# Optimization experiments

Measured on AMD Instinct MI355X. Metric: run time of the kernel, lower is better.

The kernel has to match this reference:

```python
import jax, jax.numpy as jnp
import numpy as np

PAD = 1
K = 3  # kernel_size


def conv2d(x, w, b):
    y = jax.lax.conv_general_dilated(
        x, w, window_strides=(1, 1), padding=((PAD, PAD), (PAD, PAD)),
        dimension_numbers=("NCHW", "OIHW", "NCHW"))
    return y + b[None, :, None, None]


def deform_conv2d(x, offset, weight, bias):
    # torchvision.ops.deform_conv2d semantics (stride=1, dilation=1, 1 offset group)
    B, C, H, W = x.shape
    O = weight.shape[0]
    K2 = K * K
    off = offset.reshape(B, K2, 2, H, W)  # [...,0]=dy, [...,1]=dx
    ky, kx = jnp.meshgrid(jnp.arange(K), jnp.arange(K), indexing="ij")
    ky = ky.reshape(K2).astype(x.dtype)
    kx = kx.reshape(K2).astype(x.dtype)
    hh = jnp.arange(H, dtype=x.dtype)
    ww = jnp.arange(W, dtype=x.dtype)
    # sampling coords, shape [B, K2, H, W]
    py = off[:, :, 0] + ky[None, :, None, None] + hh[None, None, :, None] - PAD
    px = off[:, :, 1] + kx[None, :, None, None] + ww[None, None, None, :] - PAD

    y0 = jnp.floor(py)
    x0 = jnp.floor(px)
    wy = (py - y0)[:, None]  # [B,1,K2,H,W]
    wx = (px - x0)[:, None]

    xf = x.reshape(B, C, H * W)

    def gather(iy, ix):
        valid = (iy >= 0) & (iy < H) & (ix >= 0) & (ix < W)
        iyc = jnp.clip(iy, 0, H - 1).astype(jnp.int32)
        ixc = jnp.clip(ix, 0, W - 1).astype(jnp.int32)
        idx = (iyc * W + ixc).reshape(B, 1, K2 * H * W)
        v = jnp.take_along_axis(xf, idx, axis=2).reshape(B, C, K2, H, W)
        return v * valid.reshape(B, 1, K2, H, W).astype(x.dtype)

    v00 = gather(y0, x0)
    v01 = gather(y0, x0 + 1)
    v10 = gather(y0 + 1, x0)
    v11 = gather(y0 + 1, x0 + 1)
    sampled = (v00 * (1 - wy) * (1 - wx) + v01 * (1 - wy) * wx
               + v10 * wy * (1 - wx) + v11 * wy * wx)  # [B,C,K2,H,W]
    out = jnp.einsum("bckhw,ock->bohw", sampled, weight.reshape(O, C, K2))
    return out + bias[None, :, None, None]


def setup_inputs() -> dict:
    key = jax.random.key(0)
    k1, k2, k3, k4, k5 = jax.random.split(key, 5)
    B, C, H, W = 4, 64, 192, 192
    O = 64
    x = jax.random.normal(k1, (B, C, H, W), dtype=jnp.float32)
    w_off = jax.random.normal(k2, (2 * K * K, C, K, K), dtype=jnp.float32) * 0.05
    b_off = jnp.zeros((2 * K * K,), dtype=jnp.float32)
    w_conv = jax.random.normal(k3, (O, C, K, K), dtype=jnp.float32) * (1.0 / np.sqrt(C * K * K))
    b_conv = jax.random.normal(k4, (O,), dtype=jnp.float32) * 0.01
    return {"x": x, "w_off": w_off, "b_off": b_off, "w_conv": w_conv, "b_conv": b_conv}


def reference(x, w_off, b_off, w_conv, b_conv):
    offset = conv2d(x, w_off, b_off)
    y = deform_conv2d(x, offset, w_conv, b_conv)
    return conv2d(y, w_conv, b_conv)  # module reuses self.conv on deform output
```

## Files before the change

### kernel.cpp

```cpp
#include <hip/hip_runtime.h>

constexpr int B = 4;
constexpr int C = 64;
constexpr int O = 64;
constexpr int OOFF = 18;
constexpr int H = 192;
constexpr int W = 192;

typedef __attribute__((ext_vector_type(8))) _Float16 half8;
typedef __attribute__((ext_vector_type(2))) _Float16 h16x2;
typedef __attribute__((ext_vector_type(4))) float float4v;

__device__ inline ushort f2h(float f) {
  return __builtin_bit_cast(ushort, (_Float16)f);
}
__device__ inline uint pk2h(float lo, float hi) {
  h16x2 v;
  v.x = (_Float16)lo;
  v.y = (_Float16)hi;
  return __builtin_bit_cast(uint, v);
}

__global__ __launch_bounds__(256) void k_pre(const float* __restrict__ x,
                                             ushort* __restrict__ xtf,
                                             const float* __restrict__ w_conv,
                                             ushort* __restrict__ wBf,
                                             const float* __restrict__ w_off,
                                             ushort* __restrict__ wOf) {
  __shared__ float tile[64][17];
  const int bid = blockIdx.x;
  const int tid = threadIdx.x;
  if (bid < 9216) {
    const int w0 = (bid % 12) * 16;
    const int h = (bid / 12) % 192;
    const int b = bid / 2304;
    const int wl = tid & 15;
    const int c0 = tid >> 4;
#pragma unroll
    for (int r = 0; r < 4; ++r) {
      const int c = c0 + r * 16;
      tile[c][wl] = x[(((size_t)b * C + c) * H + h) * W + w0 + wl];
    }
    __syncthreads();
    const int c = tid & 63;
    const int qq = tid >> 6;
#pragma unroll
    for (int r = 0; r < 4; ++r) {
      const int wq = qq + r * 4;
      xtf[(((size_t)b * H + h) * W + w0 + wq) * C + c] = f2h(tile[c][wq]);
    }
  } else if (bid < 9360) {
    const int i = (bid - 9216) * 256 + tid;
    const int j = i & 7;
    const int lane = (i >> 3) & 63;
    const int nt = (i >> 9) & 3;
    const int kstep = (i >> 11) & 1;
    const int kk = i >> 12;
    const int n = nt + 4 * (lane & 15);
    const int c = kstep * 32 + ((lane >> 4) & 3) * 8 + j;
    wBf[i] = f2h(w_conv[((size_t)n * C + c) * 9 + kk]);
  } else {
    const int i = (bid - 9360) * 256 + tid;
    const int j = i & 7;
    const int lane = (i >> 3) & 63;
    const int nt = (i >> 9) & 1;
    const int ks = (i >> 10) & 1;
    const int kk = i >> 11;
    const int n = nt * 16 + (lane & 15);
    const int c = ks * 32 + ((lane >> 4) & 3) * 8 + j;
    wOf[i] = (n < OOFF) ? f2h(w_off[((size_t)n * C + c) * 9 + kk]) : (ushort)0;
  }
}

__global__ __launch_bounds__(256) void k_fused(
    const ushort* __restrict__ xtf, const ushort* __restrict__ wOf,
    const float* __restrict__ b_off, const ushort* __restrict__ wBf,
    const float* __restrict__ b_conv, ushort* __restrict__ yt) {
  __shared__ ushort sA[4][2][64][8];
  __shared__ __align__(16) float offBuf[4][16][20];

  const int bid = blockIdx.x;
  const int xcd = bid & 7;
  const int s = bid >> 3;
  const int b = xcd >> 1;
  const int half = xcd & 1;
  const int th = half * 12 + s / 24;
  const int tw = s % 24;
  const int h0 = th * 8, w0 = tw * 8;

  const int tid = threadIdx.x;
  const int wave = tid >> 6, lane = tid & 63;
  const int col = lane & 15, quad = lane >> 4;
  const int p = tid >> 2, qtr = tid & 3;
  const int pl = p & 15;
  const int prow = p >> 3, pcol = p & 7;
  const int h = h0 + prow, w = w0 + pcol;
  const int ks_w = qtr >> 1;
  const int q2 = (qtr & 1) * 2;

  {
    float4v oacc[2];
#pragma unroll
    for (int nt = 0; nt < 2; ++nt) oacc[nt] = (float4v){0.f, 0.f, 0.f, 0.f};

    half8 obfr[2][2][2];
    half8 oafr[2][2];

    auto oload = [&](int kk, int pb) {
      const int ky = kk / 3, kx = kk % 3;
      const int hh = h0 + 2 * wave + (col >> 3) + ky - 1;
      const int ww = w0 + (col & 7) + kx - 1;
      const bool ok = ((unsigned)hh < (unsigned)H) && ((unsigned)ww < (unsigned)W);
      const int hhc = min(max(hh, 0), H - 1);
      const int wwc = min(max(ww, 0), W - 1);
      const ushort* pa = xtf + (((size_t)b * H + hhc) * W + wwc) * C + quad * 8;
#pragma unroll
      for (int ks = 0; ks < 2; ++ks) {
        half8 v = (half8)0;
        if (ok) v = *(const half8*)(pa + ks * 32);
        oafr[pb][ks] = v;
#pragma unroll
        for (int nt = 0; nt < 2; ++nt)
          obfr[pb][ks][nt] = *(const half8*)&wOf[((((size_t)kk * 2 + ks) * 2 + nt) * 64 + lane) * 8];
      }
    };

    oload(0, 0);
#pragma unroll
    for (int kk = 0; kk < 9; ++kk) {
      const int pb = kk & 1;
      if (kk < 8) oload(kk + 1, pb ^ 1);
#pragma unroll
      for (int ks = 0; ks < 2; ++ks)
#pragma unroll
        for (int nt = 0; nt < 2; ++nt)
          oacc[nt] = __builtin_amdgcn_mfma_f32_16x16x32_f16(oafr[pb][ks], obfr[pb][ks][nt],
                                                            oacc[nt], 0, 0, 0);
    }

#pragma unroll
    for (int nt = 0; nt < 2; ++nt) {
      const int oc = nt * 16 + col;
      if (oc < OOFF) {
        const float bias = b_off[oc];
#pragma unroll
        for (int r = 0; r < 4; ++r)
          offBuf[wave][quad * 4 + r][oc] = oacc[nt][r] + bias;
      }
    }
  }

  float2 offv[9];
#pragma unroll
  for (int kk = 0; kk < 9; ++kk) offv[kk] = *(const float2*)&offBuf[wave][pl][2 * kk];

  const ushort* xb = xtf + (size_t)b * H * W * C + qtr * 16;

  uint4 G[3][8];
  float4 aw[3];

  auto issue = [&](int kk, int buf) {
    const float dy = offv[kk].x, dx = offv[kk].y;
    const int ky = kk / 3, kx = kk % 3;
    const float pyf = dy + (float)(ky + h - 1);
    const float pxf = dx + (float)(kx + w - 1);
    const float fy0 = floorf(pyf), fx0 = floorf(pxf);
    const float wy = pyf - fy0, wx = pxf - fx0;
    const int iy0 = (int)fy0, ix0 = (int)fx0;
    const int iy1 = iy0 + 1, ix1 = ix0 + 1;
    const bool vy0 = (unsigned)iy0 < (unsigned)H;
    const bool vy1 = (unsigned)iy1 < (unsigned)H;
    const bool vx0 = (unsigned)ix0 < (unsigned)W;
    const bool vx1 = (unsigned)ix1 < (unsigned)W;
    aw[buf].x = (vy0 && vx0) ? (1.f - wy) * (1.f - wx) : 0.f;
    aw[buf].y = (vy0 && vx1) ? (1.f - wy) * wx : 0.f;
    aw[buf].z = (vy1 && vx0) ? wy * (1.f - wx) : 0.f;
    aw[buf].w = (vy1 && vx1) ? wy * wx : 0.f;
    const int cy0 = min(max(iy0, 0), H - 1), cy1 = min(max(iy1, 0), H - 1);
    const int cx0 = min(max(ix0, 0), W - 1), cx1 = min(max(ix1, 0), W - 1);
    const uint4* p00 = (const uint4*)(xb + ((size_t)cy0 * W + cx0) * C);
    const uint4* p01 = (const uint4*)(xb + ((size_t)cy0 * W + cx1) * C);
    const uint4* p10 = (const uint4*)(xb + ((size_t)cy1 * W + cx0) * C);
    const uint4* p11 = (const uint4*)(xb + ((size_t)cy1 * W + cx1) * C);
    G[buf][0] = p00[0]; G[buf][1] = p00[1];
    G[buf][2] = p01[0]; G[buf][3] = p01[1];
    G[buf][4] = p10[0]; G[buf][5] = p10[1];
    G[buf][6] = p11[0]; G[buf][7] = p11[1];
  };

  float4v acc[4];
#pragma unroll
  for (int nt = 0; nt < 4; ++nt) acc[nt] = (float4v){0.f, 0.f, 0.f, 0.f};

  issue(0, 0);
  issue(1, 1);
#pragma unroll
  for (int kk = 0; kk < 9; ++kk) {
    const int buf = kk % 3;
    if (kk < 7) issue(kk + 2, (kk + 2) % 3);

    const _Float16 w00 = (_Float16)aw[buf].x, w01 = (_Float16)aw[buf].y;
    const _Float16 w10 = (_Float16)aw[buf].z, w11 = (_Float16)aw[buf].w;
    const h16x2 a00 = {w00, w00}, a01 = {w01, w01}, a10 = {w10, w10}, a11 = {w11, w11};
    uint pk[8];
#pragma unroll
    for (int i = 0; i < 8; ++i) {
      const h16x2 v00 = __builtin_bit_cast(h16x2, ((const uint*)&G[buf][0])[i]);
      const h16x2 v01 = __builtin_bit_cast(h16x2, ((const uint*)&G[buf][2])[i]);
      const h16x2 v10 = __builtin_bit_cast(h16x2, ((const uint*)&G[buf][4])[i]);
      const h16x2 v11 = __builtin_bit_cast(h16x2, ((const uint*)&G[buf][6])[i]);
      const h16x2 sv = v00 * a00 + v01 * a01 + v10 * a10 + v11 * a11;
      pk[i] = __builtin_bit_cast(uint, sv);
    }
    *(uint4*)&sA[wave][ks_w][pl | (q2 << 4)][0] = *(const uint4*)&pk[0];
    *(uint4*)&sA[wave][ks_w][pl | ((q2 + 1) << 4)][0] = *(const uint4*)&pk[4];

#pragma unroll
    for (int ks = 0; ks < 2; ++ks) {
      const half8 a = *(const half8*)&sA[wave][ks][lane][0];
#pragma unroll
      for (int nt = 0; nt < 4; ++nt) {
        const half8 bb = *(const half8*)&wBf[((((size_t)kk * 2 + ks) * 4 + nt) * 64 + lane) * 8];
        acc[nt] = __builtin_amdgcn_mfma_f32_16x16x32_f16(a, bb, acc[nt], 0, 0, 0);
      }
    }
  }

  float bias[4];
#pragma unroll
  for (int nt = 0; nt < 4; ++nt) bias[nt] = b_conv[4 * col + nt];
#pragma unroll
  for (int r = 0; r < 4; ++r) {
    const int pp = wave * 16 + quad * 4 + r;
    const int hrow = h0 + (pp >> 3), wcol = w0 + (pp & 7);
    uint2 u;
    u.x = pk2h(acc[0][r] + bias[0], acc[1][r] + bias[1]);
    u.y = pk2h(acc[2][r] + bias[2], acc[3][r] + bias[3]);
    *(uint2*)&yt[((size_t)(b * H + hrow) * W + wcol) * C + 4 * col] = u;
  }
}

__global__ __launch_bounds__(256) void k_conv_main_mfma(
    const ushort* __restrict__ yt, const ushort* __restrict__ wBf,
    const float* __restrict__ b_conv, float* __restrict__ out) {
  const int w0 = blockIdx.x * 16;
  const int b = blockIdx.z;
  const int tid = threadIdx.x;
  const int wave = tid >> 6, lane = tid & 63;
  const int col = lane & 15, quad = lane >> 4;
  const int h0 = blockIdx.y * 16 + wave * 4;

  float4v acc[4][4];
#pragma unroll
  for (int mt = 0; mt < 4; ++mt)
#pragma unroll
    for (int nt = 0; nt < 4; ++nt) acc[mt][nt] = (float4v){0.f, 0.f, 0.f, 0.f};

  half8 bfr[2][2][4];
  half8 afr[2][4][2];

  auto load = [&](int kk, int pb) {
    const int ky = kk / 3, kx = kk % 3;
    const int ww = w0 + col + kx - 1;
    const bool wok = (unsigned)ww < (unsigned)W;
    const int wwc = min(max(ww, 0), W - 1);
#pragma unroll
    for (int ks = 0; ks < 2; ++ks)
#pragma unroll
      for (int nt = 0; nt < 4; ++nt)
        bfr[pb][ks][nt] = *(const half8*)&wBf[((((size_t)kk * 2 + ks) * 4 + nt) * 64 + lane) * 8];
#pragma unroll
    for (int mt = 0; mt < 4; ++mt) {
      const int hh = h0 + mt + ky - 1;
      const bool ok = wok && ((unsigned)hh < (unsigned)H);
      const int hhc = min(max(hh, 0), H - 1);
      const ushort* pa = yt + (((size_t)b * H + hhc) * W + wwc) * C + quad * 8;
#pragma unroll
      for (int ks = 0; ks < 2; ++ks) {
        half8 v = (half8)0;
        if (ok) v = *(const half8*)(pa + ks * 32);
        afr[pb][mt][ks] = v;
      }
    }
  };

  load(0, 0);
#pragma unroll
  for (int kk = 0; kk < 9; ++kk) {
    const int pb = kk & 1;
    if (kk < 8) load(kk + 1, pb ^ 1);
#pragma unroll
    for (int ks = 0; ks < 2; ++ks)
#pragma unroll
      for (int mt = 0; mt < 4; ++mt)
#pragma unroll
        for (int nt = 0; nt < 4; ++nt)
          acc[mt][nt] = __builtin_amdgcn_mfma_f32_16x16x32_f16(afr[pb][mt][ks], bfr[pb][ks][nt],
                                                               acc[mt][nt], 0, 0, 0);
  }

  float bias[4];
#pragma unroll
  for (int nt = 0; nt < 4; ++nt) bias[nt] = b_conv[4 * col + nt];
#pragma unroll
  for (int mt = 0; mt < 4; ++mt) {
    const int h = h0 + mt;
#pragma unroll
    for (int nt = 0; nt < 4; ++nt) {
      const int oc = 4 * col + nt;
      float4 v;
      v.x = acc[mt][nt][0] + bias[nt];
      v.y = acc[mt][nt][1] + bias[nt];
      v.z = acc[mt][nt][2] + bias[nt];
      v.w = acc[mt][nt][3] + bias[nt];
      *(float4*)&out[(((size_t)b * O + oc) * H + h) * W + w0 + quad * 4] = v;
    }
  }
}

extern "C" void kernel_launch(void* const* d_in, const int* in_sizes, int n_in,
                              void* d_out, int out_size, void* d_ws, size_t ws_size,
                              hipStream_t stream) {
  const float* x = (const float*)d_in[0];
  const float* w_off = (const float*)d_in[1];
  const float* b_off = (const float*)d_in[2];
  const float* w_conv = (const float*)d_in[3];
  const float* b_conv = (const float*)d_in[4];
  float* out = (float*)d_out;

  ushort* xtf = (ushort*)d_ws;
  ushort* yt = xtf + (size_t)B * H * W * C;
  ushort* wBf = yt + (size_t)B * H * W * C;
  ushort* wOf = wBf + 36864;

  const dim3 blk(256);
  k_pre<<<dim3(9432), blk, 0, stream>>>(x, xtf, w_conv, wBf, w_off, wOf);
  k_fused<<<dim3(2304), blk, 0, stream>>>(xtf, wOf, b_off, wBf, b_conv, yt);
  k_conv_main_mfma<<<dim3(W / 16, H / 16, B), blk, 0, stream>>>(yt, wBf, b_conv, out);
}
```

Baseline: 203.3 us.

## Gather deform samples directly into MFMA A-fragment layout and halve conv tile rows

In the fused deformable kernel, each lane now handles one pixel (col) and one 8-channel slice per ks (quad), so the bilinear-interpolated values land directly in the MFMA A-operand layout. This removes the shared-memory staging buffer sA and its store/reload round trip. Each of the 4 lanes in a pixel group now repeats the offset and weight math, and the gather loads shrink to 16 bytes. Separately, the final conv kernel uses 2 rows per wave instead of 4, doubling the grid for more occupancy at the cost of less weight reuse per block.

```diff
diff --git a/kernel.cpp b/kernel.cpp
--- a/kernel.cpp
+++ b/kernel.cpp
@@ -76,7 +76,6 @@
     const ushort* __restrict__ xtf, const ushort* __restrict__ wOf,
     const float* __restrict__ b_off, const ushort* __restrict__ wBf,
     const float* __restrict__ b_conv, ushort* __restrict__ yt) {
-  __shared__ ushort sA[4][2][64][8];
   __shared__ __align__(16) float offBuf[4][16][20];
 
   const int bid = blockIdx.x;
@@ -91,12 +90,9 @@
   const int tid = threadIdx.x;
   const int wave = tid >> 6, lane = tid & 63;
   const int col = lane & 15, quad = lane >> 4;
-  const int p = tid >> 2, qtr = tid & 3;
-  const int pl = p & 15;
-  const int prow = p >> 3, pcol = p & 7;
-  const int h = h0 + prow, w = w0 + pcol;
-  const int ks_w = qtr >> 1;
-  const int q2 = (qtr & 1) * 2;
+
+  const int pp = wave * 16 + col;
+  const int ph = h0 + (pp >> 3), pw = w0 + (pp & 7);
 
   {
     float4v oacc[2];
@@ -108,8 +104,8 @@
 
     auto oload = [&](int kk, int pb) {
       const int ky = kk / 3, kx = kk % 3;
-      const int hh = h0 + 2 * wave + (col >> 3) + ky - 1;
-      const int ww = w0 + (col & 7) + kx - 1;
+      const int hh = ph + ky - 1;
+      const int ww = pw + kx - 1;
       const bool ok = ((unsigned)hh < (unsigned)H) && ((unsigned)ww < (unsigned)W);
       const int hhc = min(max(hh, 0), H - 1);
       const int wwc = min(max(ww, 0), W - 1);
@@ -150,20 +146,17 @@
     }
   }
 
-  float2 offv[9];
-#pragma unroll
-  for (int kk = 0; kk < 9; ++kk) offv[kk] = *(const float2*)&offBuf[wave][pl][2 * kk];
-
-  const ushort* xb = xtf + (size_t)b * H * W * C + qtr * 16;
-
-  uint4 G[3][8];
+  const ushort* xq = xtf + (size_t)b * H * W * C + quad * 8;
+
+  half8 G[3][8];
   float4 aw[3];
 
   auto issue = [&](int kk, int buf) {
-    const float dy = offv[kk].x, dx = offv[kk].y;
+    const float2 ov = *(const float2*)&offBuf[wave][col][2 * kk];
+    const float dy = ov.x, dx = ov.y;
     const int ky = kk / 3, kx = kk % 3;
-    const float pyf = dy + (float)(ky + h - 1);
-    const float pxf = dx + (float)(kx + w - 1);
+    const float pyf = dy + (float)(ky + ph - 1);
+    const float pxf = dx + (float)(kx + pw - 1);
     const float fy0 = floorf(pyf), fx0 = floorf(pxf);
     const float wy = pyf - fy0, wx = pxf - fx0;
     const int iy0 = (int)fy0, ix0 = (int)fx0;
@@ -178,14 +171,14 @@
     aw[buf].w = (vy1 && vx1) ? wy * wx : 0.f;
     const int cy0 = min(max(iy0, 0), H - 1), cy1 = min(max(iy1, 0), H - 1);
     const int cx0 = min(max(ix0, 0), W - 1), cx1 = min(max(ix1, 0), W - 1);
-    const uint4* p00 = (const uint4*)(xb + ((size_t)cy0 * W + cx0) * C);
-    const uint4* p01 = (const uint4*)(xb + ((size_t)cy0 * W + cx1) * C);
-    const uint4* p10 = (const uint4*)(xb + ((size_t)cy1 * W + cx0) * C);
-    const uint4* p11 = (const uint4*)(xb + ((size_t)cy1 * W + cx1) * C);
-    G[buf][0] = p00[0]; G[buf][1] = p00[1];
-    G[buf][2] = p01[0]; G[buf][3] = p01[1];
-    G[buf][4] = p10[0]; G[buf][5] = p10[1];
-    G[buf][6] = p11[0]; G[buf][7] = p11[1];
+    const ushort* p00 = xq + ((size_t)cy0 * W + cx0) * C;
+    const ushort* p01 = xq + ((size_t)cy0 * W + cx1) * C;
+    const ushort* p10 = xq + ((size_t)cy1 * W + cx0) * C;
+    const ushort* p11 = xq + ((size_t)cy1 * W + cx1) * C;
+    G[buf][0] = *(const half8*)(p00);      G[buf][1] = *(const half8*)(p00 + 32);
+    G[buf][2] = *(const half8*)(p01);      G[buf][3] = *(const half8*)(p01 + 32);
+    G[buf][4] = *(const half8*)(p10);      G[buf][5] = *(const half8*)(p10 + 32);
+    G[buf][6] = *(const half8*)(p11);      G[buf][7] = *(const half8*)(p11 + 32);
   };
 
   float4v acc[4];
@@ -201,29 +194,19 @@
 
     const _Float16 w00 = (_Float16)aw[buf].x, w01 = (_Float16)aw[buf].y;
     const _Float16 w10 = (_Float16)aw[buf].z, w11 = (_Float16)aw[buf].w;
-    const h16x2 a00 = {w00, w00}, a01 = {w01, w01}, a10 = {w10, w10}, a11 = {w11, w11};
-    uint pk[8];
-#pragma unroll
-    for (int i = 0; i < 8; ++i) {
-      const h16x2 v00 = __builtin_bit_cast(h16x2, ((const uint*)&G[buf][0])[i]);
-      const h16x2 v01 = __builtin_bit_cast(h16x2, ((const uint*)&G[buf][2])[i]);
-      const h16x2 v10 = __builtin_bit_cast(h16x2, ((const uint*)&G[buf][4])[i]);
-      const h16x2 v11 = __builtin_bit_cast(h16x2, ((const uint*)&G[buf][6])[i]);
-      const h16x2 sv = v00 * a00 + v01 * a01 + v10 * a10 + v11 * a11;
-      pk[i] = __builtin_bit_cast(uint, sv);
-    }
-    *(uint4*)&sA[wave][ks_w][pl | (q2 << 4)][0] = *(const uint4*)&pk[0];
-    *(uint4*)&sA[wave][ks_w][pl | ((q2 + 1) << 4)][0] = *(const uint4*)&pk[4];
-
-#pragma unroll
-    for (int ks = 0; ks < 2; ++ks) {
-      const half8 a = *(const half8*)&sA[wave][ks][lane][0];
+    half8 af[2];
+#pragma unroll
+    for (int ks = 0; ks < 2; ++ks)
+      af[ks] = G[buf][0 + ks] * w00 + G[buf][2 + ks] * w01 +
+               G[buf][4 + ks] * w10 + G[buf][6 + ks] * w11;
+
+#pragma unroll
+    for (int ks = 0; ks < 2; ++ks)
 #pragma unroll
       for (int nt = 0; nt < 4; ++nt) {
         const half8 bb = *(const half8*)&wBf[((((size_t)kk * 2 + ks) * 4 + nt) * 64 + lane) * 8];
-        acc[nt] = __builtin_amdgcn_mfma_f32_16x16x32_f16(a, bb, acc[nt], 0, 0, 0);
+        acc[nt] = __builtin_amdgcn_mfma_f32_16x16x32_f16(af[ks], bb, acc[nt], 0, 0, 0);
       }
-    }
   }
 
   float bias[4];
@@ -231,8 +214,8 @@
   for (int nt = 0; nt < 4; ++nt) bias[nt] = b_conv[4 * col + nt];
 #pragma unroll
   for (int r = 0; r < 4; ++r) {
-    const int pp = wave * 16 + quad * 4 + r;
-    const int hrow = h0 + (pp >> 3), wcol = w0 + (pp & 7);
+    const int pe = wave * 16 + quad * 4 + r;
+    const int hrow = h0 + (pe >> 3), wcol = w0 + (pe & 7);
     uint2 u;
     u.x = pk2h(acc[0][r] + bias[0], acc[1][r] + bias[1]);
     u.y = pk2h(acc[2][r] + bias[2], acc[3][r] + bias[3]);
@@ -248,16 +231,16 @@
   const int tid = threadIdx.x;
   const int wave = tid >> 6, lane = tid & 63;
   const int col = lane & 15, quad = lane >> 4;
-  const int h0 = blockIdx.y * 16 + wave * 4;
-
-  float4v acc[4][4];
-#pragma unroll
-  for (int mt = 0; mt < 4; ++mt)
+  const int h0 = blockIdx.y * 8 + wave * 2;
+
+  float4v acc[2][4];
+#pragma unroll
+  for (int mt = 0; mt < 2; ++mt)
 #pragma unroll
     for (int nt = 0; nt < 4; ++nt) acc[mt][nt] = (float4v){0.f, 0.f, 0.f, 0.f};
 
   half8 bfr[2][2][4];
-  half8 afr[2][4][2];
+  half8 afr[2][2][2];
 
   auto load = [&](int kk, int pb) {
     const int ky = kk / 3, kx = kk % 3;
@@ -270,7 +253,7 @@
       for (int nt = 0; nt < 4; ++nt)
         bfr[pb][ks][nt] = *(const half8*)&wBf[((((size_t)kk * 2 + ks) * 4 + nt) * 64 + lane) * 8];
 #pragma unroll
-    for (int mt = 0; mt < 4; ++mt) {
+    for (int mt = 0; mt < 2; ++mt) {
       const int hh = h0 + mt + ky - 1;
       const bool ok = wok && ((unsigned)hh < (unsigned)H);
       const int hhc = min(max(hh, 0), H - 1);
@@ -292,7 +275,7 @@
 #pragma unroll
     for (int ks = 0; ks < 2; ++ks)
 #pragma unroll
-      for (int mt = 0; mt < 4; ++mt)
+      for (int mt = 0; mt < 2; ++mt)
 #pragma unroll
         for (int nt = 0; nt < 4; ++nt)
           acc[mt][nt] = __builtin_amdgcn_mfma_f32_16x16x32_f16(afr[pb][mt][ks], bfr[pb][ks][nt],
@@ -303,7 +286,7 @@
 #pragma unroll
   for (int nt = 0; nt < 4; ++nt) bias[nt] = b_conv[4 * col + nt];
 #pragma unroll
-  for (int mt = 0; mt < 4; ++mt) {
+  for (int mt = 0; mt < 2; ++mt) {
     const int h = h0 + mt;
 #pragma unroll
     for (int nt = 0; nt < 4; ++nt) {
@@ -336,5 +319,5 @@
   const dim3 blk(256);
   k_pre<<<dim3(9432), blk, 0, stream>>>(x, xtf, w_conv, wBf, w_off, wOf);
   k_fused<<<dim3(2304), blk, 0, stream>>>(xtf, wOf, b_off, wBf, b_conv, yt);
-  k_conv_main_mfma<<<dim3(W / 16, H / 16, B), blk, 0, stream>>>(yt, wBf, b_conv, out);
-}
+  k_conv_main_mfma<<<dim3(W / 16, H / 8, B), blk, 0, stream>>>(yt, wBf, b_conv, out);
+}
```

Result: slower. 246.2 us (+21.1%).
